# Kernel tuning notes

Hardware: AMD Instinct MI355X
Metric: run time of the kernel (lower is better)

## Reference

```python
import jax, jax.numpy as jnp
import numpy as np
import math

B, S, C, H = 32, 500, 1024, 16
D = C // H  # head dim = 64

def setup_inputs() -> dict:
    key = jax.random.key(0)
    ks = jax.random.split(key, 9)
    sc = 1.0 / math.sqrt(C)
    return {
        "x": jax.random.normal(ks[0], (B, S, C), dtype=jnp.float32),
        "Wq": jax.random.normal(ks[1], (C, C), dtype=jnp.float32) * sc,
        "bq": jnp.zeros((C,), dtype=jnp.float32),
        "Wk": jax.random.normal(ks[2], (C, C), dtype=jnp.float32) * sc,
        "bk": jnp.zeros((C,), dtype=jnp.float32),
        "Wv": jax.random.normal(ks[3], (C, C), dtype=jnp.float32) * sc,
        "bv": jnp.zeros((C,), dtype=jnp.float32),
        "Wp": jax.random.normal(ks[4], (C, C), dtype=jnp.float32) * sc,
        "bp": jnp.zeros((C,), dtype=jnp.float32),
    }

def reference(x, Wq, bq, Wk, bk, Wv, bv, Wp, bp):
    # Projections -> [B, H, S, D]
    q = (x @ Wq + bq).reshape(B, S, H, D).transpose(0, 2, 1, 3)
    k = (x @ Wk + bk).reshape(B, S, H, D).transpose(0, 2, 1, 3)
    v = (x @ Wv + bv).reshape(B, S, H, D).transpose(0, 2, 1, 3)
    # Scaled scores [B, H, S, S]
    att = jnp.einsum('bhqd,bhkd->bhqk', q, k) * (1.0 / math.sqrt(D))
    causal = jnp.tril(jnp.ones((S, S), dtype=bool))
    att = jnp.where(causal[None, None], att, jnp.float32(-1e10))
    att = jax.nn.softmax(att, axis=-1)
    # (dropout is identity in eval mode)
    y = jnp.einsum('bhqk,bhkd->bhqd', att, v)  # [B, H, S, D]
    y = y.transpose(0, 2, 1, 3).reshape(B, S, C)
    return y @ Wp + bp
```

## Files before the change

### kernel.cpp

```cpp
#include <hip/hip_runtime.h>
#include <math.h>

#define B_ 32
#define S_ 500
#define C_ 1024
#define H_ 16
#define D_ 64
#define M_ (B_ * S_)
#define SP 512

typedef _Float16 f16;
typedef f16 f16x8 __attribute__((ext_vector_type(8)));
typedef f16 f16x4 __attribute__((ext_vector_type(4)));
typedef float f32x4 __attribute__((ext_vector_type(4)));

#define GLOBAL_AS __attribute__((address_space(1)))
#define LDS_AS __attribute__((address_space(3)))

__device__ __forceinline__ void async_load16(const void* g, void* l) {
    __builtin_amdgcn_global_load_lds((const GLOBAL_AS void*)g, (LDS_AS void*)l, 16, 0, 0);
}

struct MaskF { static constexpr bool value = false; };
struct MaskT { static constexpr bool value = true; };

__global__ __launch_bounds__(256) void cast_rows(
    const float* __restrict__ in, f16* __restrict__ out, int n8)
{
    int i = blockIdx.x * 256 + threadIdx.x;
    if (i >= n8) return;
    float4 a = ((const float4*)in)[2 * i];
    float4 b = ((const float4*)in)[2 * i + 1];
    f16x8 h;
    h[0] = (f16)a.x; h[1] = (f16)a.y; h[2] = (f16)a.z; h[3] = (f16)a.w;
    h[4] = (f16)b.x; h[5] = (f16)b.y; h[6] = (f16)b.z; h[7] = (f16)b.w;
    ((f16x8*)out)[i] = h;
}

__global__ __launch_bounds__(256) void castW_T(
    const float* __restrict__ W, f16* __restrict__ T)
{
    __shared__ float t[32][33];
    const int n0 = blockIdx.x * 32, k0 = blockIdx.y * 32;
    const int tx = threadIdx.x, ty = threadIdx.y;
#pragma unroll
    for (int i = 0; i < 4; ++i)
        t[ty + 8 * i][tx] = W[(size_t)(k0 + ty + 8 * i) * C_ + n0 + tx];
    __syncthreads();
#pragma unroll
    for (int i = 0; i < 4; ++i) {
        int n = ty + 8 * i;
        T[(size_t)(n0 + n) * C_ + k0 + tx] = (f16)t[tx][n];
    }
}

template <int MODE>
__global__ __launch_bounds__(256) void gemm_mfma(
    const f16* __restrict__ A, const f16* __restrict__ W,
    const float* __restrict__ bias, void* __restrict__ out0, float oscale)
{
    constexpr int K = C_, N = C_;
    __shared__ __align__(16) f16 sA[128 * 32];
    __shared__ __align__(16) f16 sW[128 * 32];

    const int tid = threadIdx.x;
    const int lin = blockIdx.y * 8 + blockIdx.x;
    const int bid = (lin & 7) * 125 + (lin >> 3);
    const int m0 = (bid >> 3) * 128;
    const int n0 = (bid & 7) * 128;
    const int lane = tid & 63;
    const int w = tid >> 6;
    const int wm = (w & 1) * 64;
    const int wn = (w >> 1) * 64;
    const int quad = lane >> 4;
    const int lr = lane & 15;

    const f16* gA[2];
    const f16* gW[2];
    f16* lA[2];
    f16* lW[2];
#pragma unroll
    for (int p = 0; p < 2; ++p) {
        int slot = p * 256 + tid;
        int row = slot >> 2, c = slot & 3;
        int csw = c ^ ((row >> 1) & 3);
        gA[p] = A + (size_t)(m0 + row) * K + csw * 8;
        gW[p] = W + (size_t)(n0 + row) * K + csw * 8;
        lA[p] = &sA[slot * 8];
        lW[p] = &sW[slot * 8];
    }

    f32x4 acc[4][4];
#pragma unroll
    for (int i = 0; i < 4; ++i)
#pragma unroll
        for (int j = 0; j < 4; ++j) acc[i][j] = (f32x4)0.f;

    int offA[4], offB[4];
#pragma unroll
    for (int t = 0; t < 4; ++t) {
        int m = wm + t * 16 + lr;
        offA[t] = m * 32 + (quad ^ ((m >> 1) & 3)) * 8;
        int n = wn + t * 16 + lr;
        offB[t] = n * 32 + (quad ^ ((n >> 1) & 3)) * 8;
    }

    for (int k0 = 0; k0 < K; k0 += 32) {
#pragma unroll
        for (int p = 0; p < 2; ++p) {
            async_load16(gA[p] + k0, lA[p]);
            async_load16(gW[p] + k0, lW[p]);
        }
        __syncthreads();

        f16x8 af[4], bf[4];
#pragma unroll
        for (int t = 0; t < 4; ++t) {
            af[t] = *(const f16x8*)&sA[offA[t]];
            bf[t] = *(const f16x8*)&sW[offB[t]];
        }
#pragma unroll
        for (int mt = 0; mt < 4; ++mt)
#pragma unroll
            for (int nt = 0; nt < 4; ++nt)
                acc[mt][nt] = __builtin_amdgcn_mfma_f32_16x16x32_f16(
                    af[mt], bf[nt], acc[mt][nt], 0, 0, 0);
        __syncthreads();
    }

#pragma unroll
    for (int nt = 0; nt < 4; ++nt) {
        int gc = n0 + wn + nt * 16 + lr;
        float bv = bias[gc];
        int h = gc >> 6, d = gc & 63;
#pragma unroll
        for (int mt = 0; mt < 4; ++mt) {
            int gr0 = m0 + wm + mt * 16 + quad * 4;
            int b = gr0 / S_, s0 = gr0 - b * S_;
            if (MODE == 0) {
                f16* oq = (f16*)out0;
#pragma unroll
                for (int r = 0; r < 4; ++r) {
                    float v = (acc[mt][nt][r] + bv) * oscale;
                    size_t idx = (((size_t)b * H_ + h) * S_ + (s0 + r)) * D_ + d;
                    oq[idx] = (f16)v;
                }
            } else if (MODE == 2) {
                f16* ov = (f16*)out0;
                f16x4 pk;
#pragma unroll
                for (int r = 0; r < 4; ++r) pk[r] = (f16)(acc[mt][nt][r] + bv);
                *(f16x4*)(ov + (((size_t)b * H_ + h) * D_ + d) * SP + s0) = pk;
            } else {
                float* of = (float*)out0;
#pragma unroll
                for (int r = 0; r < 4; ++r)
                    of[(size_t)(gr0 + r) * N + gc] = acc[mt][nt][r] + bv;
            }
        }
    }
}

__global__ __launch_bounds__(256) void attn_mfma(
    const f16* __restrict__ qg, const f16* __restrict__ kg,
    const f16* __restrict__ vt, f16* __restrict__ Y)
{
    __shared__ __align__(16) f16 sK[64 * 64];
    __shared__ __align__(16) f16 sVt[64 * 64];
    __shared__ __align__(16) f16 sP[4 * 32 * 64];

    const int tid = threadIdx.x;
    const int lin = blockIdx.y * 4 + blockIdx.x;
    const int bid = (lin & 7) * 256 + (lin >> 3);
    const int qt = bid & 3, bh = bid >> 2;
    const int q0 = qt * 128;
    const int lane = tid & 63, w = tid >> 6;
    const int quad = lane >> 4, lr = lane & 15;
    const size_t gbase = (size_t)bh * S_ * D_;
    const size_t vbase = (size_t)bh * D_ * SP;
    const int psw = (lr & 7) << 1;

    f16x8 qf[2][2];
#pragma unroll
    for (int t = 0; t < 2; ++t) {
        int q = q0 + w * 32 + t * 16 + lr;
        const f16* pq = qg + gbase + (size_t)q * D_;
#pragma unroll
        for (int s2 = 0; s2 < 2; ++s2)
            qf[t][s2] = *(const f16x8*)(pq + quad * 8 + 32 * s2);
    }

    f32x4 accO[2][4];
#pragma unroll
    for (int t = 0; t < 2; ++t)
#pragma unroll
        for (int nt = 0; nt < 4; ++nt) accO[t][nt] = (f32x4)0.f;
    float l_run[2] = {0.f, 0.f};

    auto iter = [&](int kt, auto masked_tag) __attribute__((always_inline)) {
        constexpr bool MASKED = decltype(masked_tag)::value;
        const int k0 = kt * 64;
#pragma unroll
        for (int it = 0; it < 2; ++it) {
            int idx = it * 256 + tid;
            int row = idx >> 3, c = idx & 7;
            int csw = (c ^ (row & 7)) * 8;
            async_load16(kg + gbase + (size_t)(k0 + row) * D_ + csw, &sK[idx * 8]);
            async_load16(vt + vbase + (size_t)row * SP + k0 + csw, &sVt[idx * 8]);
        }
        __syncthreads();

        f32x4 accS[4][2];
#pragma unroll
        for (int mt = 0; mt < 4; ++mt)
#pragma unroll
            for (int t = 0; t < 2; ++t) accS[mt][t] = (f32x4)0.f;
#pragma unroll
        for (int mt = 0; mt < 4; ++mt) {
            int row = mt * 16 + lr;
#pragma unroll
            for (int s2 = 0; s2 < 2; ++s2) {
                int off = row * 64 + (((quad + 4 * s2) ^ (lr & 7)) << 3);
                f16x8 ka = *(const f16x8*)&sK[off];
#pragma unroll
                for (int t = 0; t < 2; ++t)
                    accS[mt][t] = __builtin_amdgcn_mfma_f32_16x16x32_f16(
                        ka, qf[t][s2], accS[mt][t], 0, 0, 0);
            }
        }

        float ls[2] = {0.f, 0.f};
#pragma unroll
        for (int mt = 0; mt < 4; ++mt)
#pragma unroll
            for (int t = 0; t < 2; ++t) {
                f16x4 pk;
#pragma unroll
                for (int r = 0; r < 4; ++r) {
                    float s = accS[mt][t][r];
                    if (MASKED) {
                        int key = k0 + mt * 16 + quad * 4 + r;
                        int qq = q0 + w * 32 + t * 16 + lr;
                        s = (key <= qq && key < S_) ? s : -1e30f;
                    }
                    float p = __expf(s);
                    ls[t] += p;
                    pk[r] = (f16)p;
                }
                int c8 = (mt * 4 + quad) ^ psw;
                *(f16x4*)&sP[w * 2048 + (t * 16 + lr) * 64 + c8 * 4] = pk;
            }
        ls[0] += __shfl_xor(ls[0], 16); ls[0] += __shfl_xor(ls[0], 32);
        ls[1] += __shfl_xor(ls[1], 16); ls[1] += __shfl_xor(ls[1], 32);
        l_run[0] += ls[0];
        l_run[1] += ls[1];

#pragma unroll
        for (int t = 0; t < 2; ++t) {
            int pb = w * 2048 + (t * 16 + lr) * 64;
#pragma unroll
            for (int s2 = 0; s2 < 2; ++s2) {
                int c8 = (quad * 2 + 8 * s2) ^ psw;
                f16x8 pf = *(const f16x8*)&sP[pb + c8 * 4];
#pragma unroll
                for (int nt = 0; nt < 4; ++nt) {
                    f16x8 vf = *(const f16x8*)
                        &sVt[(nt * 16 + lr) * 64 + (((quad + 4 * s2) ^ (lr & 7)) << 3)];
                    accO[t][nt] = __builtin_amdgcn_mfma_f32_16x16x32_f16(
                        pf, vf, accO[t][nt], 0, 0, 0);
                }
            }
        }
        __syncthreads();
    };

    for (int kt = 0; kt < 2 * qt; ++kt) iter(kt, MaskF{});
    iter(2 * qt, MaskT{});
    iter(2 * qt + 1, MaskT{});

    const int b = bh >> 4, h = bh & 15;
#pragma unroll
    for (int t = 0; t < 2; ++t) {
#pragma unroll
        for (int r = 0; r < 4; ++r) {
            float lsum = __shfl(l_run[t], quad * 4 + r);
            float iv = 1.f / lsum;
            int s = q0 + w * 32 + t * 16 + quad * 4 + r;
            if (s >= S_) continue;
            size_t rowbase = (size_t)(b * S_ + s) * C_ + h * 64;
#pragma unroll
            for (int nt = 0; nt < 4; ++nt)
                Y[rowbase + nt * 16 + lr] = (f16)(accO[t][nt][r] * iv);
        }
    }
}

extern "C" void kernel_launch(void* const* d_in, const int* in_sizes, int n_in,
                              void* d_out, int out_size, void* d_ws, size_t ws_size,
                              hipStream_t stream)
{
    const float* x = (const float*)d_in[0];
    const float* Wq = (const float*)d_in[1];
    const float* bq = (const float*)d_in[2];
    const float* Wk = (const float*)d_in[3];
    const float* bk = (const float*)d_in[4];
    const float* Wv = (const float*)d_in[5];
    const float* bv = (const float*)d_in[6];
    const float* Wp = (const float*)d_in[7];
    const float* bp = (const float*)d_in[8];

    const size_t NEL = (size_t)M_ * C_;
    const size_t WEL = (size_t)C_ * C_;
    f16* qf = (f16*)d_ws;
    f16* kf = qf + NEL;
    f16* vt = kf + NEL;
    f16* xf = vt + (size_t)B_ * H_ * D_ * SP;
    f16* wpf = xf + NEL;
    f16* yf = xf;

    f16* wq = (f16*)d_out;
    f16* wk = wq + WEL;
    f16* wv = wk + WEL;

    dim3 tg(32, 32), tb(32, 8);
    castW_T<<<tg, tb, 0, stream>>>(Wq, wq);
    castW_T<<<tg, tb, 0, stream>>>(Wk, wk);
    castW_T<<<tg, tb, 0, stream>>>(Wv, wv);
    castW_T<<<tg, tb, 0, stream>>>(Wp, wpf);

    int n8 = (int)(NEL / 8);
    cast_rows<<<(n8 + 255) / 256, 256, 0, stream>>>(x, xf, n8);

    dim3 gg(8, 125), bb(256);
    gemm_mfma<0><<<gg, bb, 0, stream>>>(xf, wq, bq, qf, 0.125f);
    gemm_mfma<0><<<gg, bb, 0, stream>>>(xf, wk, bk, kf, 1.0f);
    gemm_mfma<2><<<gg, bb, 0, stream>>>(xf, wv, bv, vt, 1.0f);

    attn_mfma<<<dim3(4, B_ * H_), bb, 0, stream>>>(qf, kf, vt, yf);

    gemm_mfma<1><<<gg, bb, 0, stream>>>(yf, wpf, bp, d_out, 1.0f);
}
```

Measured before the change: 408.6 us.

## Fuse QKV projections into one GEMM launch and double-buffer K/V in attention

```diff
diff --git a/kernel.cpp b/kernel.cpp
--- a/kernel.cpp
+++ b/kernel.cpp
@@ -57,17 +57,21 @@
 template <int MODE>
 __global__ __launch_bounds__(256) void gemm_mfma(
     const f16* __restrict__ A, const f16* __restrict__ W,
-    const float* __restrict__ bias, void* __restrict__ out0, float oscale)
-{
-    constexpr int K = C_, N = C_;
+    const float* __restrict__ b0, const float* __restrict__ b1,
+    const float* __restrict__ b2, void* __restrict__ o0,
+    void* __restrict__ o1, void* __restrict__ o2)
+{
+    constexpr int K = C_;
+    constexpr int NB = (MODE == 0) ? 24 : 8;
+    constexpr int CHUNK = (NB * 125) / 8;
     __shared__ __align__(16) f16 sA[128 * 32];
     __shared__ __align__(16) f16 sW[128 * 32];
 
     const int tid = threadIdx.x;
-    const int lin = blockIdx.y * 8 + blockIdx.x;
-    const int bid = (lin & 7) * 125 + (lin >> 3);
-    const int m0 = (bid >> 3) * 128;
-    const int n0 = (bid & 7) * 128;
+    const int lin = blockIdx.x;
+    const int bid = (lin & 7) * CHUNK + (lin >> 3);
+    const int m0 = (bid / NB) * 128;
+    const int n0 = (bid % NB) * 128;
     const int lane = tid & 63;
     const int w = tid >> 6;
     const int wm = (w & 1) * 64;
@@ -131,31 +135,42 @@
 #pragma unroll
     for (int nt = 0; nt < 4; ++nt) {
         int gc = n0 + wn + nt * 16 + lr;
-        float bv = bias[gc];
-        int h = gc >> 6, d = gc & 63;
-#pragma unroll
-        for (int mt = 0; mt < 4; ++mt) {
-            int gr0 = m0 + wm + mt * 16 + quad * 4;
-            int b = gr0 / S_, s0 = gr0 - b * S_;
-            if (MODE == 0) {
-                f16* oq = (f16*)out0;
-#pragma unroll
-                for (int r = 0; r < 4; ++r) {
-                    float v = (acc[mt][nt][r] + bv) * oscale;
-                    size_t idx = (((size_t)b * H_ + h) * S_ + (s0 + r)) * D_ + d;
-                    oq[idx] = (f16)v;
+        if (MODE == 1) {
+            float bv = b0[gc];
+            float* of = (float*)o0;
+#pragma unroll
+            for (int mt = 0; mt < 4; ++mt) {
+                int gr0 = m0 + wm + mt * 16 + quad * 4;
+#pragma unroll
+                for (int r = 0; r < 4; ++r)
+                    of[(size_t)(gr0 + r) * C_ + gc] = acc[mt][nt][r] + bv;
+            }
+        } else {
+            int sec = gc >> 10;
+            int gcl = gc & 1023;
+            const float* bp = (sec == 0) ? b0 : (sec == 1) ? b1 : b2;
+            float bv = bp[gcl];
+            float osc = (sec == 0) ? 0.125f : 1.0f;
+            int h = gcl >> 6, d = gcl & 63;
+#pragma unroll
+            for (int mt = 0; mt < 4; ++mt) {
+                int gr0 = m0 + wm + mt * 16 + quad * 4;
+                int b = gr0 / S_, s0 = gr0 - b * S_;
+                if (sec < 2) {
+                    f16* oq = (f16*)((sec == 0) ? o0 : o1);
+#pragma unroll
+                    for (int r = 0; r < 4; ++r) {
+                        float v = (acc[mt][nt][r] + bv) * osc;
+                        size_t idx = (((size_t)b * H_ + h) * S_ + (s0 + r)) * D_ + d;
+                        oq[idx] = (f16)v;
+                    }
+                } else {
+                    f16* ov = (f16*)o2;
+                    f16x4 pk;
+#pragma unroll
+                    for (int r = 0; r < 4; ++r) pk[r] = (f16)(acc[mt][nt][r] + bv);
+                    *(f16x4*)(ov + (((size_t)b * H_ + h) * D_ + d) * SP + s0) = pk;
                 }
-            } else if (MODE == 2) {
-                f16* ov = (f16*)out0;
-                f16x4 pk;
-#pragma unroll
-                for (int r = 0; r < 4; ++r) pk[r] = (f16)(acc[mt][nt][r] + bv);
-                *(f16x4*)(ov + (((size_t)b * H_ + h) * D_ + d) * SP + s0) = pk;
-            } else {
-                float* of = (float*)out0;
-#pragma unroll
-                for (int r = 0; r < 4; ++r)
-                    of[(size_t)(gr0 + r) * N + gc] = acc[mt][nt][r] + bv;
             }
         }
     }
@@ -165,14 +180,16 @@
     const f16* __restrict__ qg, const f16* __restrict__ kg,
     const f16* __restrict__ vt, f16* __restrict__ Y)
 {
-    __shared__ __align__(16) f16 sK[64 * 64];
-    __shared__ __align__(16) f16 sVt[64 * 64];
+    __shared__ __align__(16) f16 sK[2][64 * 64];
+    __shared__ __align__(16) f16 sVt[2][64 * 64];
     __shared__ __align__(16) f16 sP[4 * 32 * 64];
 
     const int tid = threadIdx.x;
-    const int lin = blockIdx.y * 4 + blockIdx.x;
-    const int bid = (lin & 7) * 256 + (lin >> 3);
-    const int qt = bid & 3, bh = bid >> 2;
+    const int lin = blockIdx.x;
+    const int xcd = lin & 7;
+    const int pos = lin >> 3;
+    const int bh = xcd * 64 + (pos >> 2);
+    const int qt = 3 - (pos & 3);
     const int q0 = qt * 128;
     const int lane = tid & 63, w = tid >> 6;
     const int quad = lane >> 4, lr = lane & 15;
@@ -197,18 +214,25 @@
         for (int nt = 0; nt < 4; ++nt) accO[t][nt] = (f32x4)0.f;
     float l_run[2] = {0.f, 0.f};
 
-    auto iter = [&](int kt, auto masked_tag) __attribute__((always_inline)) {
-        constexpr bool MASKED = decltype(masked_tag)::value;
+    const int NT = 2 * qt + 2;
+
+    auto stage = [&](int kt, int buf) __attribute__((always_inline)) {
         const int k0 = kt * 64;
 #pragma unroll
         for (int it = 0; it < 2; ++it) {
             int idx = it * 256 + tid;
             int row = idx >> 3, c = idx & 7;
             int csw = (c ^ (row & 7)) * 8;
-            async_load16(kg + gbase + (size_t)(k0 + row) * D_ + csw, &sK[idx * 8]);
-            async_load16(vt + vbase + (size_t)row * SP + k0 + csw, &sVt[idx * 8]);
-        }
-        __syncthreads();
+            async_load16(kg + gbase + (size_t)(k0 + row) * D_ + csw, &sK[buf][idx * 8]);
+            async_load16(vt + vbase + (size_t)row * SP + k0 + csw, &sVt[buf][idx * 8]);
+        }
+    };
+
+    auto step = [&](int kt, auto masked_tag) __attribute__((always_inline)) {
+        constexpr bool MASKED = decltype(masked_tag)::value;
+        const int cur = kt & 1;
+        if (kt + 1 < NT) stage(kt + 1, cur ^ 1);
+        const int k0 = kt * 64;
 
         f32x4 accS[4][2];
 #pragma unroll
@@ -221,7 +245,7 @@
 #pragma unroll
             for (int s2 = 0; s2 < 2; ++s2) {
                 int off = row * 64 + (((quad + 4 * s2) ^ (lr & 7)) << 3);
-                f16x8 ka = *(const f16x8*)&sK[off];
+                f16x8 ka = *(const f16x8*)&sK[cur][off];
 #pragma unroll
                 for (int t = 0; t < 2; ++t)
                     accS[mt][t] = __builtin_amdgcn_mfma_f32_16x16x32_f16(
@@ -265,7 +289,7 @@
 #pragma unroll
                 for (int nt = 0; nt < 4; ++nt) {
                     f16x8 vf = *(const f16x8*)
-                        &sVt[(nt * 16 + lr) * 64 + (((quad + 4 * s2) ^ (lr & 7)) << 3)];
+                        &sVt[cur][(nt * 16 + lr) * 64 + (((quad + 4 * s2) ^ (lr & 7)) << 3)];
                     accO[t][nt] = __builtin_amdgcn_mfma_f32_16x16x32_f16(
                         pf, vf, accO[t][nt], 0, 0, 0);
                 }
@@ -274,9 +298,11 @@
         __syncthreads();
     };
 
-    for (int kt = 0; kt < 2 * qt; ++kt) iter(kt, MaskF{});
-    iter(2 * qt, MaskT{});
-    iter(2 * qt + 1, MaskT{});
+    stage(0, 0);
+    __syncthreads();
+    for (int kt = 0; kt < 2 * qt; ++kt) step(kt, MaskF{});
+    step(2 * qt, MaskT{});
+    step(2 * qt + 1, MaskT{});
 
     const int b = bh >> 4, h = bh & 15;
 #pragma unroll
@@ -313,8 +339,8 @@
     const size_t WEL = (size_t)C_ * C_;
     f16* qf = (f16*)d_ws;
     f16* kf = qf + NEL;
-    f16* vt = kf + NEL;
-    f16* xf = vt + (size_t)B_ * H_ * D_ * SP;
+    f16* vtw = kf + NEL;
+    f16* xf = vtw + (size_t)B_ * H_ * D_ * SP;
     f16* wpf = xf + NEL;
     f16* yf = xf;
 
@@ -331,12 +357,10 @@
     int n8 = (int)(NEL / 8);
     cast_rows<<<(n8 + 255) / 256, 256, 0, stream>>>(x, xf, n8);
 
-    dim3 gg(8, 125), bb(256);
-    gemm_mfma<0><<<gg, bb, 0, stream>>>(xf, wq, bq, qf, 0.125f);
-    gemm_mfma<0><<<gg, bb, 0, stream>>>(xf, wk, bk, kf, 1.0f);
-    gemm_mfma<2><<<gg, bb, 0, stream>>>(xf, wv, bv, vt, 1.0f);
-
-    attn_mfma<<<dim3(4, B_ * H_), bb, 0, stream>>>(qf, kf, vt, yf);
-
-    gemm_mfma<1><<<gg, bb, 0, stream>>>(yf, wpf, bp, d_out, 1.0f);
-}
+    gemm_mfma<0><<<3000, 256, 0, stream>>>(xf, wq, bq, bk, bv, qf, kf, vtw);
+
+    attn_mfma<<<2048, 256, 0, stream>>>(qf, kf, vtw, yf);
+
+    gemm_mfma<1><<<1000, 256, 0, stream>>>(yf, wpf, bp, nullptr, nullptr,
+                                           d_out, nullptr, nullptr);
+}
```

Measured after the change: 393.6 us. 1.04x faster.
